# Optimization experiments

Measured on AMD Instinct MI355X. Metric: run time of the kernel, lower is better.

## Reference

```python
import jax, jax.numpy as jnp
import numpy as np

H, W, D = 60, 60, 36            # voxel grid dims (x, y, z)
GRID = 0.08                      # voxel size in meters
SCALE_MULT = 3.0                 # radius multiplier
CHUNK = 7200                     # point-chunk size; 129600 / 7200 = 18 chunks
P = 2048                         # number of Gaussians
C = 13                           # semantic channels


def setup_inputs() -> dict:
    key = jax.random.key(0)
    k1, k2, k3, k4, k5 = jax.random.split(key, 5)
    # query points = voxel centers, guaranteed in-range for the int-bin asserts
    ii, jj, kk = jnp.meshgrid(jnp.arange(H), jnp.arange(W), jnp.arange(D), indexing='ij')
    pts = (jnp.stack([ii, jj, kk], axis=-1).reshape(-1, 3).astype(jnp.float32) + 0.5) * GRID
    pts = pts[None]  # [1, N, 3]
    lo = jnp.array([0.1, 0.1, 0.1], jnp.float32)
    hi = jnp.array([H, W, D], jnp.float32) * GRID - 0.1
    means3D = jax.random.uniform(k1, (1, P, 3), dtype=jnp.float32) * (hi - lo) + lo
    scales = jax.random.uniform(k2, (1, P, 3), minval=0.03, maxval=0.2, dtype=jnp.float32)
    # random rotations via QR -> SPD covariance Sigma = Q diag(s^2) Q^T
    A = jax.random.normal(k3, (P, 3, 3), dtype=jnp.float32)
    Q, _ = jnp.linalg.qr(A)
    cov3D = jnp.einsum('pij,pj,pkj->pik', Q, scales[0] ** 2, Q)[None]  # [1,P,3,3]
    opacities = jax.random.uniform(k4, (1, P), minval=0.1, maxval=1.0, dtype=jnp.float32)
    semantics = jax.random.normal(k5, (1, P, C), dtype=jnp.float32)
    origin_use = jnp.zeros((3,), jnp.float32)
    return {"pts": pts, "means3D": means3D, "opacities": opacities,
            "semantics": semantics, "scales": scales, "cov3D": cov3D,
            "origin_use": origin_use}


def _sym_inv6(packed):
    # packed: [P,6] = (xx, yy, zz, xy, yz, xz) of a symmetric 3x3 covariance
    a, b, c, d, e, f = (packed[:, i] for i in range(6))
    det = a * (b * c - e * e) - d * (d * c - e * f) + f * (d * e - b * f)
    ixx = (b * c - e * e) / det
    iyy = (a * c - f * f) / det
    izz = (a * b - d * d) / det
    ixy = (e * f - d * c) / det
    iyz = (d * f - a * e) / det
    ixz = (d * e - b * f) / det
    return ixx, iyy, izz, ixy, iyz, ixz


def _forward(pts, means3D, opacities, semantics, scales, cov3D, origin_use):
    pts = pts[0]                    # [N,3], no grad in original
    means3D = means3D[0]            # [P,3]
    opacities = opacities[0]        # [P]
    semantics = semantics[0]        # [P,C]
    scales = jax.lax.stop_gradient(scales[0])   # detached in original
    cov3D = cov3D[0]                # [P,3,3]

    radii = jnp.ceil(scales.max(-1) * SCALE_MULT / GRID).astype(jnp.int32)  # [P]
    m_int = ((jax.lax.stop_gradient(means3D) - origin_use) / GRID).astype(jnp.int32)  # [P,3]
    packed = cov3D.reshape(-1, 9)[:, jnp.array([0, 4, 8, 1, 5, 2])]  # [P,6]
    ixx, iyy, izz, ixy, iyz, ixz = _sym_inv6(packed)  # per-Gaussian inverse cov entries

    N = pts.shape[0]
    pts_c = pts.reshape(N // CHUNK, CHUNK, 3)

    def chunk_fn(p):  # p: [CHUNK,3]
        p_int = ((p - origin_use) / GRID).astype(jnp.int32)
        dx = p[:, 0:1] - means3D[None, :, 0]   # [CHUNK,P]
        dy = p[:, 1:2] - means3D[None, :, 1]
        dz = p[:, 2:3] - means3D[None, :, 2]
        quad = (ixx * dx * dx + iyy * dy * dy + izz * dz * dz
                + 2.0 * (ixy * dx * dy + iyz * dy * dz + ixz * dx * dz))
        inbox = (jnp.abs(p_int[:, None, :] - m_int[None, :, :])
                 <= radii[None, :, None]).all(-1)          # [CHUNK,P] box/bin test
        w = jnp.where(inbox, opacities[None, :] * jnp.exp(-0.5 * quad), 0.0)
        return w @ semantics                                # [CHUNK,C]

    logits = jax.lax.map(chunk_fn, pts_c).reshape(N, C)
    return logits


def reference(pts, means3D, opacities, semantics, scales, cov3D, origin_use):
    return _forward(pts, means3D, opacities, semantics, scales, cov3D, origin_use)
```

## Files before the change

kernel.cpp:

```cpp
#include <hip/hip_runtime.h>


constexpr int   HH      = 60;
constexpr int   WW      = 60;
constexpr int   DD      = 36;
constexpr int   P_N     = 2048;
constexpr int   C_N     = 13;
constexpr int   REC     = 24;
constexpr int   BXD     = 15;
constexpr int   BYD     = 15;
constexpr int   BZD     = 9;
constexpr int   NBRICK  = BXD * BYD * BZD;
constexpr int   MAXL    = 256;
constexpr float GRID_SZ = 0.08f;

__global__ void precompute_kernel(const float* __restrict__ means,
                                  const float* __restrict__ opac,
                                  const float* __restrict__ sem,
                                  const float* __restrict__ scales,
                                  const float* __restrict__ cov,
                                  const float* __restrict__ origin,
                                  float* __restrict__ recs,
                                  int4* __restrict__ boxes) {
    int g = blockIdx.x * blockDim.x + threadIdx.x;
    if (g >= P_N) return;
    float mx = means[g * 3 + 0], my = means[g * 3 + 1], mz = means[g * 3 + 2];
    float sx = scales[g * 3 + 0], sy = scales[g * 3 + 1], sz = scales[g * 3 + 2];
    float smax = fmaxf(sx, fmaxf(sy, sz));
    int rad = (int)ceilf(smax * 3.0f / GRID_SZ);
    float ox = origin[0], oy = origin[1], oz = origin[2];
    int mix = (int)((mx - ox) / GRID_SZ);
    int miy = (int)((my - oy) / GRID_SZ);
    int miz = (int)((mz - oz) / GRID_SZ);
    const float* cv = cov + g * 9;
    float a = cv[0], b = cv[4], c = cv[8], d = cv[1], e = cv[5], f = cv[2];
    float det = a * (b * c - e * e) - d * (d * c - e * f) + f * (d * e - b * f);
    const float kD = -0.5f * 1.44269504088896340736f;
    const float kO = -1.44269504088896340736f;
    float* r = recs + g * REC;
    r[0] = mx; r[1] = my; r[2] = mz;
    r[3] = __log2f(opac[g]);
    r[4] = kD * (b * c - e * e) / det;
    r[5] = kD * (a * c - f * f) / det;
    r[6] = kD * (a * b - d * d) / det;
    r[7] = kO * (e * f - d * c) / det;
    r[8] = kO * (d * f - a * e) / det;
    r[9] = kO * (d * e - b * f) / det;
#pragma unroll
    for (int cc = 0; cc < C_N; ++cc) r[10 + cc] = sem[g * C_N + cc];
    r[23] = 0.0f;
    boxes[g] = make_int4(mix, miy, miz, rad);
}

__global__ __launch_bounds__(256) void agg_kernel(const float* __restrict__ recs,
                                                  const int4* __restrict__ boxes,
                                                  float* __restrict__ out) {
    __shared__ int   s_idx[MAXL];
    __shared__ int   s_cnt;
    __shared__ float s_acc[4][64][C_N];

    const int b = (int)blockIdx.x;
    const int bk = b % BZD; const int rem = b / BZD;
    const int bj = rem % BYD; const int bi = rem / BYD;
    const int i0 = bi * 4, j0 = bj * 4, k0 = bk * 4;

    if (threadIdx.x == 0) s_cnt = 0;
    __syncthreads();

    for (int g = (int)threadIdx.x; g < P_N; g += 256) {
        int4 bx = boxes[g];
        bool ov = (bx.x - bx.w <= i0 + 3) && (bx.x + bx.w >= i0)
               && (bx.y - bx.w <= j0 + 3) && (bx.y + bx.w >= j0)
               && (bx.z - bx.w <= k0 + 3) && (bx.z + bx.w >= k0);
        if (ov) {
            int xlo = max(bx.x - bx.w - i0, 0), xhi = min(bx.x + bx.w - i0, 3);
            int ylo = max(bx.y - bx.w - j0, 0), yhi = min(bx.y + bx.w - j0, 3);
            int zlo = max(bx.z - bx.w - k0, 0), zhi = min(bx.z + bx.w - k0, 3);
            unsigned mx4 = (0xFu >> (3 - xhi)) & (0xFu << xlo);
            unsigned my4 = (0xFu >> (3 - yhi)) & (0xFu << ylo);
            unsigned mz4 = (0xFu >> (3 - zhi)) & (0xFu << zlo);
            unsigned ent = (unsigned)g | (mx4 << 12) | (my4 << 16) | (mz4 << 20);
            int t = atomicAdd(&s_cnt, 1);
            if (t < MAXL) s_idx[t] = (int)ent;
        }
    }
    __syncthreads();
    const int cnt = min(s_cnt, MAXL);

    const int wave = (int)threadIdx.x >> 6;
    const int lane = (int)threadIdx.x & 63;
    const int kk = lane & 3, lj = (lane >> 2) & 3, li = lane >> 4;
    const int gi = i0 + li, gj = j0 + lj, k = k0 + kk;
    const float px = ((float)gi + 0.5f) * GRID_SZ;
    const float py = ((float)gj + 0.5f) * GRID_SZ;
    const float pz = ((float)k  + 0.5f) * GRID_SZ;
    const unsigned sel = (1u << (12 + li)) | (1u << (16 + lj)) | (1u << (20 + kk));

    float acc[C_N];
#pragma unroll
    for (int cc = 0; cc < C_N; ++cc) acc[cc] = 0.0f;

#pragma unroll 2
    for (int i = wave; i < cnt; i += 4) {
        const unsigned ent = (unsigned)s_idx[i];
        const int g = (int)(ent & 0xFFFu);
        const float4* __restrict__ rp = (const float4*)(recs + (long)g * REC);
        const float4 r0 = rp[0];
        const float4 r1 = rp[1];
        const float4 r2 = rp[2];
        const float4 r3 = rp[3];
        const float4 r4 = rp[4];
        const float4 r5 = rp[5];
        const bool inbox = (ent & sel) == sel;
        const float dx = px - r0.x, dy = py - r0.y, dz = pz - r0.z;
        float e2 = r0.w;
        e2 = fmaf(r1.x, dx * dx, e2);
        e2 = fmaf(r1.y, dy * dy, e2);
        e2 = fmaf(r1.z, dz * dz, e2);
        e2 = fmaf(r1.w, dx * dy, e2);
        e2 = fmaf(r2.x, dy * dz, e2);
        e2 = fmaf(r2.y, dx * dz, e2);
        float w = __builtin_amdgcn_exp2f(e2);
        w = inbox ? w : 0.0f;
        acc[0]  = fmaf(w, r2.z, acc[0]);
        acc[1]  = fmaf(w, r2.w, acc[1]);
        acc[2]  = fmaf(w, r3.x, acc[2]);
        acc[3]  = fmaf(w, r3.y, acc[3]);
        acc[4]  = fmaf(w, r3.z, acc[4]);
        acc[5]  = fmaf(w, r3.w, acc[5]);
        acc[6]  = fmaf(w, r4.x, acc[6]);
        acc[7]  = fmaf(w, r4.y, acc[7]);
        acc[8]  = fmaf(w, r4.z, acc[8]);
        acc[9]  = fmaf(w, r4.w, acc[9]);
        acc[10] = fmaf(w, r5.x, acc[10]);
        acc[11] = fmaf(w, r5.y, acc[11]);
        acc[12] = fmaf(w, r5.z, acc[12]);
    }

#pragma unroll
    for (int cc = 0; cc < C_N; ++cc) s_acc[wave][lane][cc] = acc[cc];
    __syncthreads();

    for (int t = (int)threadIdx.x; t < 64 * C_N; t += 256) {
        const int v = t / C_N, c = t % C_N;
        const float s = s_acc[0][v][c] + s_acc[1][v][c]
                      + s_acc[2][v][c] + s_acc[3][v][c];
        const int vk = v & 3, vj = (v >> 2) & 3, vi = v >> 4;
        const long n = (long)(i0 + vi) * (WW * DD)
                     + (long)(j0 + vj) * DD + (k0 + vk);
        out[n * C_N + c] = s;
    }
}

extern "C" void kernel_launch(void* const* d_in, const int* in_sizes, int n_in,
                              void* d_out, int out_size, void* d_ws, size_t ws_size,
                              hipStream_t stream) {
    const float* means  = (const float*)d_in[1];
    const float* opac   = (const float*)d_in[2];
    const float* sem    = (const float*)d_in[3];
    const float* scales = (const float*)d_in[4];
    const float* cov    = (const float*)d_in[5];
    const float* origin = (const float*)d_in[6];
    float* out = (float*)d_out;

    char* ws = (char*)d_ws;
    float* recs  = (float*)ws;
    int4*  boxes = (int4*)(ws + 196608);

    precompute_kernel<<<(P_N + 255) / 256, 256, 0, stream>>>(
        means, opac, sem, scales, cov, origin, recs, boxes);
    agg_kernel<<<NBRICK, 256, 0, stream>>>(recs, boxes, out);
}
```

Baseline: 98.34 us.

## Fuse per-Gaussian precompute into aggregation kernel and stage records in LDS

Removes the separate precompute launch. Each brick block now computes box overlap directly from means and scales, then computes inverse-covariance records only for the overlapping Gaussians and stages them in shared memory, so the inner loop reads LDS instead of global memory. This saves a kernel launch and the workspace round trip. In exchange, every block recomputes the bin and radius for all 2048 Gaussians plus a per-candidate matrix inverse, and the candidate cap drops from 256 to 192, which could silently truncate lists.

```diff
diff --git a/kernel.cpp b/kernel.cpp
--- a/kernel.cpp
+++ b/kernel.cpp
@@ -6,86 +6,89 @@
 constexpr int   DD      = 36;
 constexpr int   P_N     = 2048;
 constexpr int   C_N     = 13;
-constexpr int   REC     = 24;
 constexpr int   BXD     = 15;
 constexpr int   BYD     = 15;
 constexpr int   BZD     = 9;
 constexpr int   NBRICK  = BXD * BYD * BZD;
-constexpr int   MAXL    = 256;
+constexpr int   CAP     = 192;
 constexpr float GRID_SZ = 0.08f;
 
-__global__ void precompute_kernel(const float* __restrict__ means,
-                                  const float* __restrict__ opac,
-                                  const float* __restrict__ sem,
-                                  const float* __restrict__ scales,
-                                  const float* __restrict__ cov,
-                                  const float* __restrict__ origin,
-                                  float* __restrict__ recs,
-                                  int4* __restrict__ boxes) {
-    int g = blockIdx.x * blockDim.x + threadIdx.x;
-    if (g >= P_N) return;
-    float mx = means[g * 3 + 0], my = means[g * 3 + 1], mz = means[g * 3 + 2];
-    float sx = scales[g * 3 + 0], sy = scales[g * 3 + 1], sz = scales[g * 3 + 2];
-    float smax = fmaxf(sx, fmaxf(sy, sz));
-    int rad = (int)ceilf(smax * 3.0f / GRID_SZ);
-    float ox = origin[0], oy = origin[1], oz = origin[2];
-    int mix = (int)((mx - ox) / GRID_SZ);
-    int miy = (int)((my - oy) / GRID_SZ);
-    int miz = (int)((mz - oz) / GRID_SZ);
-    const float* cv = cov + g * 9;
-    float a = cv[0], b = cv[4], c = cv[8], d = cv[1], e = cv[5], f = cv[2];
-    float det = a * (b * c - e * e) - d * (d * c - e * f) + f * (d * e - b * f);
-    const float kD = -0.5f * 1.44269504088896340736f;
-    const float kO = -1.44269504088896340736f;
-    float* r = recs + g * REC;
-    r[0] = mx; r[1] = my; r[2] = mz;
-    r[3] = __log2f(opac[g]);
-    r[4] = kD * (b * c - e * e) / det;
-    r[5] = kD * (a * c - f * f) / det;
-    r[6] = kD * (a * b - d * d) / det;
-    r[7] = kO * (e * f - d * c) / det;
-    r[8] = kO * (d * f - a * e) / det;
-    r[9] = kO * (d * e - b * f) / det;
-#pragma unroll
-    for (int cc = 0; cc < C_N; ++cc) r[10 + cc] = sem[g * C_N + cc];
-    r[23] = 0.0f;
-    boxes[g] = make_int4(mix, miy, miz, rad);
-}
-
-__global__ __launch_bounds__(256) void agg_kernel(const float* __restrict__ recs,
-                                                  const int4* __restrict__ boxes,
-                                                  float* __restrict__ out) {
-    __shared__ int   s_idx[MAXL];
-    __shared__ int   s_cnt;
-    __shared__ float s_acc[4][64][C_N];
+__global__ __launch_bounds__(256) void agg_fused(const float* __restrict__ means,
+                                                 const float* __restrict__ opac,
+                                                 const float* __restrict__ sem,
+                                                 const float* __restrict__ scales,
+                                                 const float* __restrict__ cov,
+                                                 const float* __restrict__ origin,
+                                                 float* __restrict__ out) {
+    __shared__ int    s_idx[CAP];
+    __shared__ int    s_cnt;
+    __shared__ float4 s_mem[CAP * 6];
+    float (*s_acc)[64][C_N] = (float (*)[64][C_N])s_mem;
 
     const int b = (int)blockIdx.x;
     const int bk = b % BZD; const int rem = b / BZD;
     const int bj = rem % BYD; const int bi = rem / BYD;
     const int i0 = bi * 4, j0 = bj * 4, k0 = bk * 4;
 
+    const float ox = origin[0], oy = origin[1], oz = origin[2];
+
     if (threadIdx.x == 0) s_cnt = 0;
     __syncthreads();
 
     for (int g = (int)threadIdx.x; g < P_N; g += 256) {
-        int4 bx = boxes[g];
-        bool ov = (bx.x - bx.w <= i0 + 3) && (bx.x + bx.w >= i0)
-               && (bx.y - bx.w <= j0 + 3) && (bx.y + bx.w >= j0)
-               && (bx.z - bx.w <= k0 + 3) && (bx.z + bx.w >= k0);
+        const float mx = means[g * 3 + 0], my = means[g * 3 + 1], mz = means[g * 3 + 2];
+        const float sx = scales[g * 3 + 0], sy = scales[g * 3 + 1], sz = scales[g * 3 + 2];
+        const float smax = fmaxf(sx, fmaxf(sy, sz));
+        const int rad = (int)ceilf(smax * 3.0f / GRID_SZ);
+        const int mix = (int)((mx - ox) / GRID_SZ);
+        const int miy = (int)((my - oy) / GRID_SZ);
+        const int miz = (int)((mz - oz) / GRID_SZ);
+        const bool ov = (mix - rad <= i0 + 3) && (mix + rad >= i0)
+                     && (miy - rad <= j0 + 3) && (miy + rad >= j0)
+                     && (miz - rad <= k0 + 3) && (miz + rad >= k0);
         if (ov) {
-            int xlo = max(bx.x - bx.w - i0, 0), xhi = min(bx.x + bx.w - i0, 3);
-            int ylo = max(bx.y - bx.w - j0, 0), yhi = min(bx.y + bx.w - j0, 3);
-            int zlo = max(bx.z - bx.w - k0, 0), zhi = min(bx.z + bx.w - k0, 3);
+            int xlo = max(mix - rad - i0, 0), xhi = min(mix + rad - i0, 3);
+            int ylo = max(miy - rad - j0, 0), yhi = min(miy + rad - j0, 3);
+            int zlo = max(miz - rad - k0, 0), zhi = min(miz + rad - k0, 3);
             unsigned mx4 = (0xFu >> (3 - xhi)) & (0xFu << xlo);
             unsigned my4 = (0xFu >> (3 - yhi)) & (0xFu << ylo);
             unsigned mz4 = (0xFu >> (3 - zhi)) & (0xFu << zlo);
             unsigned ent = (unsigned)g | (mx4 << 12) | (my4 << 16) | (mz4 << 20);
             int t = atomicAdd(&s_cnt, 1);
-            if (t < MAXL) s_idx[t] = (int)ent;
+            if (t < CAP) s_idx[t] = (int)ent;
         }
     }
     __syncthreads();
-    const int cnt = min(s_cnt, MAXL);
+    const int cnt = min(s_cnt, CAP);
+
+    for (int e = (int)threadIdx.x; e < cnt; e += 256) {
+        const int ent = s_idx[e];
+        const int g = ent & 0xFFF;
+        const float* cv = cov + g * 9;
+        const float a = cv[0], bb = cv[4], c = cv[8], d = cv[1], e5 = cv[5], f = cv[2];
+        const float det = a * (bb * c - e5 * e5) - d * (d * c - e5 * f)
+                        + f * (d * e5 - bb * f);
+        const float kD = -0.5f * 1.44269504088896340736f;
+        const float kO = -1.44269504088896340736f;
+        float4 r0, r1, r2, r3, r4, r5;
+        r0.x = means[g * 3 + 0]; r0.y = means[g * 3 + 1]; r0.z = means[g * 3 + 2];
+        r0.w = __log2f(opac[g]);
+        r1.x = kD * (bb * c - e5 * e5) / det;
+        r1.y = kD * (a * c - f * f) / det;
+        r1.z = kD * (a * bb - d * d) / det;
+        r1.w = kO * (e5 * f - d * c) / det;
+        r2.x = kO * (d * f - a * e5) / det;
+        r2.y = kO * (d * e5 - bb * f) / det;
+        const float* sm = sem + g * C_N;
+        r2.z = sm[0];  r2.w = sm[1];
+        r3.x = sm[2];  r3.y = sm[3];  r3.z = sm[4];  r3.w = sm[5];
+        r4.x = sm[6];  r4.y = sm[7];  r4.z = sm[8];  r4.w = sm[9];
+        r5.x = sm[10]; r5.y = sm[11]; r5.z = sm[12];
+        r5.w = __int_as_float(ent);
+        float4* dst = &s_mem[e * 6];
+        dst[0] = r0; dst[1] = r1; dst[2] = r2; dst[3] = r3; dst[4] = r4; dst[5] = r5;
+    }
+    __syncthreads();
 
     const int wave = (int)threadIdx.x >> 6;
     const int lane = (int)threadIdx.x & 63;
@@ -102,15 +105,13 @@
 
 #pragma unroll 2
     for (int i = wave; i < cnt; i += 4) {
-        const unsigned ent = (unsigned)s_idx[i];
-        const int g = (int)(ent & 0xFFFu);
-        const float4* __restrict__ rp = (const float4*)(recs + (long)g * REC);
-        const float4 r0 = rp[0];
-        const float4 r1 = rp[1];
-        const float4 r2 = rp[2];
-        const float4 r3 = rp[3];
-        const float4 r4 = rp[4];
-        const float4 r5 = rp[5];
+        const float4 r0 = s_mem[i * 6 + 0];
+        const float4 r1 = s_mem[i * 6 + 1];
+        const float4 r2 = s_mem[i * 6 + 2];
+        const float4 r3 = s_mem[i * 6 + 3];
+        const float4 r4 = s_mem[i * 6 + 4];
+        const float4 r5 = s_mem[i * 6 + 5];
+        const unsigned ent = (unsigned)__float_as_int(r5.w);
         const bool inbox = (ent & sel) == sel;
         const float dx = px - r0.x, dy = py - r0.y, dz = pz - r0.z;
         float e2 = r0.w;
@@ -137,8 +138,9 @@
         acc[12] = fmaf(w, r5.z, acc[12]);
     }
 
+    __syncthreads();
 #pragma unroll
-    for (int cc = 0; cc < C_N; ++cc) s_acc[wave][lane][cc] = acc[cc];
+    for (int cc = 0; cc < C_N; ++cc) (*(&s_acc[wave]))[lane][cc] = acc[cc];
     __syncthreads();
 
     for (int t = (int)threadIdx.x; t < 64 * C_N; t += 256) {
@@ -163,11 +165,6 @@
     const float* origin = (const float*)d_in[6];
     float* out = (float*)d_out;
 
-    char* ws = (char*)d_ws;
-    float* recs  = (float*)ws;
-    int4*  boxes = (int4*)(ws + 196608);
-
-    precompute_kernel<<<(P_N + 255) / 256, 256, 0, stream>>>(
-        means, opac, sem, scales, cov, origin, recs, boxes);
-    agg_kernel<<<NBRICK, 256, 0, stream>>>(recs, boxes, out);
+    agg_fused<<<NBRICK, 256, 0, stream>>>(means, opac, sem, scales, cov,
+                                          origin, out);
 }
```

Measured after the change: 87.93 us. 1.12x faster.
